# Performance work log

Hardware: AMD Instinct MI355X
Metric: run time of the kernel (lower is better)

## Reference

```python
import jax, jax.numpy as jnp
import numpy as np


def _dequant_linear(x, wq, scale):
    # wq: int [out, in], scale: [out] per-output-channel
    w = wq.astype(jnp.float32) * scale[:, None]  # dequantize
    return jnp.einsum('bsh,oh->bso', x, w)


def setup_inputs() -> dict:
    key = jax.random.key(0)
    ks = jax.random.split(key, 7)
    B, S, H, I = 2, 2048, 4096, 14336
    x = jax.random.normal(ks[0], (B, S, H), dtype=jnp.float32)
    gate_wq = jax.random.randint(ks[1], (I, H), -128, 128, dtype=jnp.int32)
    up_wq = jax.random.randint(ks[2], (I, H), -128, 128, dtype=jnp.int32)
    down_wq = jax.random.randint(ks[3], (H, I), -128, 128, dtype=jnp.int32)
    # small positive per-channel scales (~1/(127*sqrt(fan_in)))
    gate_scale = jax.random.uniform(ks[4], (I,), dtype=jnp.float32, minval=0.5, maxval=1.5) / (127.0 * np.sqrt(H))
    up_scale = jax.random.uniform(ks[5], (I,), dtype=jnp.float32, minval=0.5, maxval=1.5) / (127.0 * np.sqrt(H))
    down_scale = jax.random.uniform(ks[6], (H,), dtype=jnp.float32, minval=0.5, maxval=1.5) / (127.0 * np.sqrt(I))
    return {'x': x, 'gate_wq': gate_wq, 'gate_scale': gate_scale,
            'up_wq': up_wq, 'up_scale': up_scale,
            'down_wq': down_wq, 'down_scale': down_scale}


def reference(x, gate_wq, gate_scale, up_wq, up_scale, down_wq, down_scale):
    gate = _dequant_linear(x, gate_wq, gate_scale)   # [B,S,I]
    up = _dequant_linear(x, up_wq, up_scale)         # [B,S,I]
    h = jax.nn.silu(gate) * up                       # SwiGLU
    return _dequant_linear(h, down_wq, down_scale)   # [B,S,H]
```

## Files before the change

kernel.cpp:

```cpp
#include <hip/hip_runtime.h>

typedef __bf16 bf16x8 __attribute__((ext_vector_type(8)));
typedef float f32x4 __attribute__((ext_vector_type(4)));

__device__ __forceinline__ unsigned short f2bf(float f) {
  unsigned u = __float_as_uint(f);
  u += 0x7FFFu + ((u >> 16) & 1u);
  return (unsigned short)(u >> 16);
}

__device__ __forceinline__ void async16(const void* g, void* l) {
  __builtin_amdgcn_global_load_lds((const __attribute__((address_space(1))) void*)g,
                                   (__attribute__((address_space(3))) void*)l,
                                   16, 0, 0);
}

__global__ void cvt_f32_bf16_k(const float4* __restrict__ in, ushort4* __restrict__ out) {
  int i = blockIdx.x * blockDim.x + threadIdx.x;
  float4 v = in[i];
  ushort4 o;
  o.x = f2bf(v.x); o.y = f2bf(v.y); o.z = f2bf(v.z); o.w = f2bf(v.w);
  out[i] = o;
}

__global__ void cvt_i32_bf16_k(const int4* __restrict__ in, ushort4* __restrict__ out) {
  int i = blockIdx.x * blockDim.x + threadIdx.x;
  int4 v = in[i];
  ushort4 o;
  o.x = f2bf((float)v.x); o.y = f2bf((float)v.y);
  o.z = f2bf((float)v.z); o.w = f2bf((float)v.w);
  out[i] = o;
}

__global__ __launch_bounds__(256, 2)
void gemm_gateup(const unsigned short* __restrict__ A,
                 const unsigned short* __restrict__ Bg,
                 const unsigned short* __restrict__ Bu,
                 const float* __restrict__ gsc, const float* __restrict__ usc,
                 unsigned short* __restrict__ Hout,
                 int M, int N, int K) {
  __shared__ unsigned short sA[128 * 64];
  __shared__ unsigned short sBg[128 * 64];
  __shared__ unsigned short sBu[128 * 64];

  const int tid  = threadIdx.x;
  const int lane = tid & 63;
  const int wv   = tid >> 6;

  const int bid = blockIdx.x;
  const int grp = bid >> 8;
  const int rem = bid & 255;
  const int bN  = ((grp << 3) + (rem & 7)) * 128;
  const int bM  = (rem >> 3) * 128;

  const int srow = lane >> 3;
  const int gcol = ((lane & 7) ^ srow) * 8;

  const unsigned short* gA  = A  + (size_t)(bM + wv * 32 + srow) * K + gcol;
  const unsigned short* gBg = Bg + (size_t)(bN + wv * 32 + srow) * K + gcol;
  const unsigned short* gBu = Bu + (size_t)(bN + wv * 32 + srow) * K + gcol;
  unsigned short* lA  = &sA [(wv * 32) * 64];
  unsigned short* lBg = &sBg[(wv * 32) * 64];
  unsigned short* lBu = &sBu[(wv * 32) * 64];

  const int r  = lane & 15;
  const int q  = lane >> 4;
  const int rx = r & 7;
  const int wm = (wv >> 1) * 64;
  const int wn = (wv & 1) * 64;

  f32x4 accg[4][4], accu[4][4];
#pragma unroll
  for (int i = 0; i < 4; i++)
#pragma unroll
    for (int j = 0; j < 4; j++) {
      accg[i][j] = f32x4{0.f, 0.f, 0.f, 0.f};
      accu[i][j] = f32x4{0.f, 0.f, 0.f, 0.f};
    }

  for (int k0 = 0; k0 < K; k0 += 64) {
    const unsigned short* pA = gA + k0;
    async16(pA,                  lA);
    async16(pA +  8 * (size_t)K, lA +  8 * 64);
    async16(pA + 16 * (size_t)K, lA + 16 * 64);
    async16(pA + 24 * (size_t)K, lA + 24 * 64);
    const unsigned short* pG = gBg + k0;
    async16(pG,                  lBg);
    async16(pG +  8 * (size_t)K, lBg +  8 * 64);
    async16(pG + 16 * (size_t)K, lBg + 16 * 64);
    async16(pG + 24 * (size_t)K, lBg + 24 * 64);
    const unsigned short* pU = gBu + k0;
    async16(pU,                  lBu);
    async16(pU +  8 * (size_t)K, lBu +  8 * 64);
    async16(pU + 16 * (size_t)K, lBu + 16 * 64);
    async16(pU + 24 * (size_t)K, lBu + 24 * 64);
    __syncthreads();

#pragma unroll
    for (int kk = 0; kk < 2; ++kk) {
      const int pc = ((kk * 4 + q) ^ rx) * 8;
      bf16x8 af[4];
#pragma unroll
      for (int mi = 0; mi < 4; mi++)
        af[mi] = *(const bf16x8*)&sA[(wm + mi * 16 + r) * 64 + pc];
#pragma unroll
      for (int ni = 0; ni < 4; ni++) {
        bf16x8 bg = *(const bf16x8*)&sBg[(wn + ni * 16 + r) * 64 + pc];
        bf16x8 bu = *(const bf16x8*)&sBu[(wn + ni * 16 + r) * 64 + pc];
#pragma unroll
        for (int mi = 0; mi < 4; mi++) {
          accg[mi][ni] = __builtin_amdgcn_mfma_f32_16x16x32_bf16(af[mi], bg, accg[mi][ni], 0, 0, 0);
          accu[mi][ni] = __builtin_amdgcn_mfma_f32_16x16x32_bf16(af[mi], bu, accu[mi][ni], 0, 0, 0);
        }
      }
    }
    __syncthreads();
  }

#pragma unroll
  for (int ni = 0; ni < 4; ni++) {
    const int col = bN + wn + ni * 16 + r;
    const float gs = gsc[col], us = usc[col];
#pragma unroll
    for (int mi = 0; mi < 4; mi++) {
#pragma unroll
      for (int rr = 0; rr < 4; rr++) {
        const int row = bM + wm + mi * 16 + q * 4 + rr;
        float g = accg[mi][ni][rr] * gs;
        float u = accu[mi][ni][rr] * us;
        float hv = (g / (1.f + __expf(-g))) * u;
        Hout[(size_t)row * N + col] = f2bf(hv);
      }
    }
  }
}

__global__ __launch_bounds__(256)
void gemm_down(const unsigned short* __restrict__ A,
               const unsigned short* __restrict__ B,
               const float* __restrict__ dsc,
               float* __restrict__ out,
               int M, int N, int K) {
  __shared__ unsigned short sA[128 * 64];
  __shared__ unsigned short sB[128 * 64];

  const int tid  = threadIdx.x;
  const int lane = tid & 63;
  const int wv   = tid >> 6;

  const int bid = blockIdx.x;
  const int grp = bid >> 9;
  const int rem = bid & 511;
  const int bN  = ((grp << 4) + (rem & 15)) * 128;
  const int bM  = (rem >> 4) * 128;

  const int srow = lane >> 3;
  const int gcol = ((lane & 7) ^ srow) * 8;

  const unsigned short* gA = A + (size_t)(bM + wv * 32 + srow) * K + gcol;
  const unsigned short* gB = B + (size_t)(bN + wv * 32 + srow) * K + gcol;
  unsigned short* lA = &sA[(wv * 32) * 64];
  unsigned short* lB = &sB[(wv * 32) * 64];

  const int r  = lane & 15;
  const int q  = lane >> 4;
  const int rx = r & 7;
  const int wm = (wv >> 1) * 64;
  const int wn = (wv & 1) * 64;

  f32x4 acc[4][4];
#pragma unroll
  for (int i = 0; i < 4; i++)
#pragma unroll
    for (int j = 0; j < 4; j++) acc[i][j] = f32x4{0.f, 0.f, 0.f, 0.f};

  for (int k0 = 0; k0 < K; k0 += 64) {
    const unsigned short* pA = gA + k0;
    async16(pA,                  lA);
    async16(pA +  8 * (size_t)K, lA +  8 * 64);
    async16(pA + 16 * (size_t)K, lA + 16 * 64);
    async16(pA + 24 * (size_t)K, lA + 24 * 64);
    const unsigned short* pB = gB + k0;
    async16(pB,                  lB);
    async16(pB +  8 * (size_t)K, lB +  8 * 64);
    async16(pB + 16 * (size_t)K, lB + 16 * 64);
    async16(pB + 24 * (size_t)K, lB + 24 * 64);
    __syncthreads();

#pragma unroll
    for (int kk = 0; kk < 2; ++kk) {
      const int pc = ((kk * 4 + q) ^ rx) * 8;
      bf16x8 af[4];
#pragma unroll
      for (int mi = 0; mi < 4; mi++)
        af[mi] = *(const bf16x8*)&sA[(wm + mi * 16 + r) * 64 + pc];
#pragma unroll
      for (int ni = 0; ni < 4; ni++) {
        bf16x8 bfr = *(const bf16x8*)&sB[(wn + ni * 16 + r) * 64 + pc];
#pragma unroll
        for (int mi = 0; mi < 4; mi++)
          acc[mi][ni] = __builtin_amdgcn_mfma_f32_16x16x32_bf16(af[mi], bfr, acc[mi][ni], 0, 0, 0);
      }
    }
    __syncthreads();
  }

#pragma unroll
  for (int ni = 0; ni < 4; ni++) {
    const int col = bN + wn + ni * 16 + r;
    const float s = dsc[col];
#pragma unroll
    for (int mi = 0; mi < 4; mi++) {
#pragma unroll
      for (int rr = 0; rr < 4; rr++) {
        const int row = bM + wm + mi * 16 + q * 4 + rr;
        out[(size_t)row * N + col] = acc[mi][ni][rr] * s;
      }
    }
  }
}

extern "C" void kernel_launch(void* const* d_in, const int* in_sizes, int n_in,
                              void* d_out, int out_size, void* d_ws, size_t ws_size,
                              hipStream_t stream) {
  constexpr int M  = 4096;
  constexpr int Hd = 4096;
  constexpr int Id = 14336;

  const float* x   = (const float*)d_in[0];
  const int*   gwq = (const int*)  d_in[1];
  const float* gsc = (const float*)d_in[2];
  const int*   uwq = (const int*)  d_in[3];
  const float* usc = (const float*)d_in[4];
  const int*   dwq = (const int*)  d_in[5];
  const float* dsc = (const float*)d_in[6];
  float* out = (float*)d_out;

  unsigned short* xb = (unsigned short*)d_ws;
  unsigned short* w0 = xb + (size_t)M * Hd;
  unsigned short* wu = w0 + (size_t)Id * Hd;
  unsigned short* hb = wu + (size_t)Id * Hd;

  cvt_f32_bf16_k<<<(M * Hd) / 1024, 256, 0, stream>>>((const float4*)x, (ushort4*)xb);
  cvt_i32_bf16_k<<<((size_t)Id * Hd) / 1024, 256, 0, stream>>>((const int4*)gwq, (ushort4*)w0);
  cvt_i32_bf16_k<<<((size_t)Id * Hd) / 1024, 256, 0, stream>>>((const int4*)uwq, (ushort4*)wu);

  gemm_gateup<<<(Id / 128) * (M / 128), 256, 0, stream>>>(xb, w0, wu, gsc, usc, hb, M, Id, Hd);

  cvt_i32_bf16_k<<<((size_t)Hd * Id) / 1024, 256, 0, stream>>>((const int4*)dwq, (ushort4*)w0);

  gemm_down<<<(Hd / 128) * (M / 128), 256, 0, stream>>>(hb, w0, dsc, out, M, Hd, Id);
}
```

Before: 2.219 ms.

## Double-buffer LDS with 8-wave 256-wide tiles and interleaved async staging

New measurement: 2.179 ms. About the same (-1.8%).

```diff
diff --git a/kernel.cpp b/kernel.cpp
--- a/kernel.cpp
+++ b/kernel.cpp
@@ -32,16 +32,43 @@
   out[i] = o;
 }
 
-__global__ __launch_bounds__(256, 2)
+#define BAR() do { asm volatile("" ::: "memory"); __builtin_amdgcn_s_barrier(); \
+                   asm volatile("" ::: "memory"); } while (0)
+
+#define STAGE2(GP, LP) do { async16((GP), (LP)); \
+    async16((GP) + 8 * (size_t)K, (LP) + 8 * 64); } while (0)
+
+#define LOAD_A(AF, CURA, HA)                                                   \
+  _Pragma("unroll") for (int mi = 0; mi < 4; ++mi)                             \
+  _Pragma("unroll") for (int kk = 0; kk < 2; ++kk)                             \
+    AF[mi][kk] = *(const bf16x8*)&(CURA)[((HA) * 128 + wrow + mi * 16 + r) * 64 \
+                                         + (((kk * 4 + q) ^ rx) * 8)];
+
+#define LOAD_B(BF, CURB, HB)                                                   \
+  _Pragma("unroll") for (int ni = 0; ni < 2; ++ni)                             \
+  _Pragma("unroll") for (int kk = 0; kk < 2; ++kk)                             \
+    BF[ni][kk] = *(const bf16x8*)&(CURB)[((HB) * 128 + wcol + ni * 16 + r) * 64 \
+                                         + (((kk * 4 + q) ^ rx) * 8)];
+
+#define MFMA16(ACC, AF, BF)                                                    \
+  __builtin_amdgcn_s_setprio(1);                                               \
+  _Pragma("unroll") for (int kk = 0; kk < 2; ++kk)                             \
+  _Pragma("unroll") for (int ni = 0; ni < 2; ++ni)                             \
+  _Pragma("unroll") for (int mi = 0; mi < 4; ++mi)                             \
+    ACC[mi][ni] = __builtin_amdgcn_mfma_f32_16x16x32_bf16(                     \
+        AF[mi][kk], BF[ni][kk], ACC[mi][ni], 0, 0, 0);                         \
+  __builtin_amdgcn_s_setprio(0);
+
+__global__ __launch_bounds__(512, 2)
 void gemm_gateup(const unsigned short* __restrict__ A,
                  const unsigned short* __restrict__ Bg,
                  const unsigned short* __restrict__ Bu,
                  const float* __restrict__ gsc, const float* __restrict__ usc,
                  unsigned short* __restrict__ Hout,
                  int M, int N, int K) {
-  __shared__ unsigned short sA[128 * 64];
-  __shared__ unsigned short sBg[128 * 64];
-  __shared__ unsigned short sBu[128 * 64];
+  __shared__ unsigned short sA [2 * 256 * 64];
+  __shared__ unsigned short sBg[2 * 128 * 64];
+  __shared__ unsigned short sBu[2 * 128 * 64];
 
   const int tid  = threadIdx.x;
   const int lane = tid & 63;
@@ -50,171 +77,241 @@
   const int bid = blockIdx.x;
   const int grp = bid >> 8;
   const int rem = bid & 255;
-  const int bN  = ((grp << 3) + (rem & 7)) * 128;
-  const int bM  = (rem >> 3) * 128;
+  const int bN  = ((grp << 4) + (rem & 15)) * 128;
+  const int bM  = (rem >> 4) * 256;
 
   const int srow = lane >> 3;
   const int gcol = ((lane & 7) ^ srow) * 8;
 
-  const unsigned short* gA  = A  + (size_t)(bM + wv * 32 + srow) * K + gcol;
-  const unsigned short* gBg = Bg + (size_t)(bN + wv * 32 + srow) * K + gcol;
-  const unsigned short* gBu = Bu + (size_t)(bN + wv * 32 + srow) * K + gcol;
-  unsigned short* lA  = &sA [(wv * 32) * 64];
-  unsigned short* lBg = &sBg[(wv * 32) * 64];
-  unsigned short* lBu = &sBu[(wv * 32) * 64];
-
-  const int r  = lane & 15;
-  const int q  = lane >> 4;
-  const int rx = r & 7;
-  const int wm = (wv >> 1) * 64;
-  const int wn = (wv & 1) * 64;
-
-  f32x4 accg[4][4], accu[4][4];
+  const unsigned short* gA0 = A  + (size_t)(bM +       wv * 16 + srow) * K + gcol;
+  const unsigned short* gA1 = A  + (size_t)(bM + 128 + wv * 16 + srow) * K + gcol;
+  const unsigned short* gBg = Bg + (size_t)(bN +       wv * 16 + srow) * K + gcol;
+  const unsigned short* gBu = Bu + (size_t)(bN +       wv * 16 + srow) * K + gcol;
+
+  const int r    = lane & 15;
+  const int q    = lane >> 4;
+  const int rx   = r & 7;
+  const int wrow = (wv >> 2) * 64;
+  const int wcol = (wv & 3) * 32;
+
+  f32x4 accg0[4][2], accg1[4][2], accu0[4][2], accu1[4][2];
 #pragma unroll
   for (int i = 0; i < 4; i++)
 #pragma unroll
-    for (int j = 0; j < 4; j++) {
-      accg[i][j] = f32x4{0.f, 0.f, 0.f, 0.f};
-      accu[i][j] = f32x4{0.f, 0.f, 0.f, 0.f};
-    }
-
-  for (int k0 = 0; k0 < K; k0 += 64) {
-    const unsigned short* pA = gA + k0;
-    async16(pA,                  lA);
-    async16(pA +  8 * (size_t)K, lA +  8 * 64);
-    async16(pA + 16 * (size_t)K, lA + 16 * 64);
-    async16(pA + 24 * (size_t)K, lA + 24 * 64);
-    const unsigned short* pG = gBg + k0;
-    async16(pG,                  lBg);
-    async16(pG +  8 * (size_t)K, lBg +  8 * 64);
-    async16(pG + 16 * (size_t)K, lBg + 16 * 64);
-    async16(pG + 24 * (size_t)K, lBg + 24 * 64);
-    const unsigned short* pU = gBu + k0;
-    async16(pU,                  lBu);
-    async16(pU +  8 * (size_t)K, lBu +  8 * 64);
-    async16(pU + 16 * (size_t)K, lBu + 16 * 64);
-    async16(pU + 24 * (size_t)K, lBu + 24 * 64);
-    __syncthreads();
-
-#pragma unroll
-    for (int kk = 0; kk < 2; ++kk) {
-      const int pc = ((kk * 4 + q) ^ rx) * 8;
-      bf16x8 af[4];
-#pragma unroll
-      for (int mi = 0; mi < 4; mi++)
-        af[mi] = *(const bf16x8*)&sA[(wm + mi * 16 + r) * 64 + pc];
-#pragma unroll
-      for (int ni = 0; ni < 4; ni++) {
-        bf16x8 bg = *(const bf16x8*)&sBg[(wn + ni * 16 + r) * 64 + pc];
-        bf16x8 bu = *(const bf16x8*)&sBu[(wn + ni * 16 + r) * 64 + pc];
-#pragma unroll
-        for (int mi = 0; mi < 4; mi++) {
-          accg[mi][ni] = __builtin_amdgcn_mfma_f32_16x16x32_bf16(af[mi], bg, accg[mi][ni], 0, 0, 0);
-          accu[mi][ni] = __builtin_amdgcn_mfma_f32_16x16x32_bf16(af[mi], bu, accu[mi][ni], 0, 0, 0);
-        }
+    for (int j = 0; j < 2; j++) {
+      accg0[i][j] = f32x4{0.f, 0.f, 0.f, 0.f};
+      accg1[i][j] = f32x4{0.f, 0.f, 0.f, 0.f};
+      accu0[i][j] = f32x4{0.f, 0.f, 0.f, 0.f};
+      accu1[i][j] = f32x4{0.f, 0.f, 0.f, 0.f};
+    }
+
+  const int NT = K >> 6;
+
+  STAGE2(gA0, &sA [ wv * 16 * 64]);
+  STAGE2(gBg, &sBg[ wv * 16 * 64]);
+  STAGE2(gBu, &sBu[ wv * 16 * 64]);
+  STAGE2(gA1, &sA [(128 + wv * 16) * 64]);
+  asm volatile("s_waitcnt vmcnt(4)" ::: "memory");
+  __builtin_amdgcn_s_barrier();
+
+  int cur = 0;
+  for (int t = 0; t < NT; ++t) {
+    const unsigned short* curA  = sA  + cur * (256 * 64);
+    const unsigned short* curBg = sBg + cur * (128 * 64);
+    const unsigned short* curBu = sBu + cur * (128 * 64);
+    unsigned short* nxtA  = sA  + (cur ^ 1) * (256 * 64);
+    unsigned short* nxtBg = sBg + (cur ^ 1) * (128 * 64);
+    unsigned short* nxtBu = sBu + (cur ^ 1) * (128 * 64);
+    const int  kn = (t + 1) << 6;
+    const bool st = (t + 1) < NT;
+
+    bf16x8 af0[4][2], af1[4][2];
+
+    {
+      bf16x8 bfr[2][2];
+      LOAD_A(af0, curA, 0);
+      LOAD_B(bfr, curBg, 0);
+      if (st) STAGE2(gA0 + kn, nxtA + wv * 16 * 64);
+      BAR();
+      MFMA16(accg0, af0, bfr);
+      if (st) asm volatile("s_waitcnt vmcnt(4)" ::: "memory");
+      else    asm volatile("s_waitcnt vmcnt(2)" ::: "memory");
+      BAR();
+    }
+    {
+      bf16x8 bfr[2][2];
+      LOAD_B(bfr, curBu, 0);
+      if (st) STAGE2(gBg + kn, nxtBg + wv * 16 * 64);
+      BAR();
+      MFMA16(accu0, af0, bfr);
+      if (st) asm volatile("s_waitcnt vmcnt(4)" ::: "memory");
+      else    asm volatile("s_waitcnt vmcnt(0)" ::: "memory");
+      BAR();
+    }
+    {
+      bf16x8 bfr[2][2];
+      LOAD_A(af1, curA, 1);
+      LOAD_B(bfr, curBg, 0);
+      if (st) STAGE2(gBu + kn, nxtBu + wv * 16 * 64);
+      BAR();
+      MFMA16(accg1, af1, bfr);
+      BAR();
+    }
+    {
+      bf16x8 bfr[2][2];
+      LOAD_B(bfr, curBu, 0);
+      if (st) STAGE2(gA1 + kn, nxtA + (128 + wv * 16) * 64);
+      BAR();
+      MFMA16(accu1, af1, bfr);
+      if (st) {
+        asm volatile("s_waitcnt vmcnt(4)" ::: "memory");
+        BAR();
       }
     }
-    __syncthreads();
+    cur ^= 1;
   }
 
 #pragma unroll
-  for (int ni = 0; ni < 4; ni++) {
-    const int col = bN + wn + ni * 16 + r;
+  for (int ni = 0; ni < 2; ++ni) {
+    const int col = bN + wcol + ni * 16 + r;
     const float gs = gsc[col], us = usc[col];
 #pragma unroll
-    for (int mi = 0; mi < 4; mi++) {
-#pragma unroll
-      for (int rr = 0; rr < 4; rr++) {
-        const int row = bM + wm + mi * 16 + q * 4 + rr;
-        float g = accg[mi][ni][rr] * gs;
-        float u = accu[mi][ni][rr] * us;
-        float hv = (g / (1.f + __expf(-g))) * u;
-        Hout[(size_t)row * N + col] = f2bf(hv);
+    for (int mi = 0; mi < 4; ++mi) {
+#pragma unroll
+      for (int rr = 0; rr < 4; ++rr) {
+        const int row0 = bM + wrow + mi * 16 + q * 4 + rr;
+        float g0 = accg0[mi][ni][rr] * gs;
+        float u0 = accu0[mi][ni][rr] * us;
+        Hout[(size_t)row0 * N + col] = f2bf((g0 / (1.f + __expf(-g0))) * u0);
+        const int row1 = row0 + 128;
+        float g1 = accg1[mi][ni][rr] * gs;
+        float u1 = accu1[mi][ni][rr] * us;
+        Hout[(size_t)row1 * N + col] = f2bf((g1 / (1.f + __expf(-g1))) * u1);
       }
     }
   }
 }
 
-__global__ __launch_bounds__(256)
+__global__ __launch_bounds__(512, 2)
 void gemm_down(const unsigned short* __restrict__ A,
                const unsigned short* __restrict__ B,
                const float* __restrict__ dsc,
                float* __restrict__ out,
                int M, int N, int K) {
-  __shared__ unsigned short sA[128 * 64];
-  __shared__ unsigned short sB[128 * 64];
+  __shared__ unsigned short sA[2 * 256 * 64];
+  __shared__ unsigned short sB[2 * 256 * 64];
 
   const int tid  = threadIdx.x;
   const int lane = tid & 63;
   const int wv   = tid >> 6;
 
-  const int bid = blockIdx.x;
-  const int grp = bid >> 9;
-  const int rem = bid & 511;
-  const int bN  = ((grp << 4) + (rem & 15)) * 128;
-  const int bM  = (rem >> 4) * 128;
+  const int bM = (blockIdx.x >> 4) * 256;
+  const int bN = (blockIdx.x & 15) * 256;
 
   const int srow = lane >> 3;
   const int gcol = ((lane & 7) ^ srow) * 8;
 
-  const unsigned short* gA = A + (size_t)(bM + wv * 32 + srow) * K + gcol;
-  const unsigned short* gB = B + (size_t)(bN + wv * 32 + srow) * K + gcol;
-  unsigned short* lA = &sA[(wv * 32) * 64];
-  unsigned short* lB = &sB[(wv * 32) * 64];
-
-  const int r  = lane & 15;
-  const int q  = lane >> 4;
-  const int rx = r & 7;
-  const int wm = (wv >> 1) * 64;
-  const int wn = (wv & 1) * 64;
-
-  f32x4 acc[4][4];
+  const unsigned short* gA0 = A + (size_t)(bM +       wv * 16 + srow) * K + gcol;
+  const unsigned short* gA1 = A + (size_t)(bM + 128 + wv * 16 + srow) * K + gcol;
+  const unsigned short* gB0 = B + (size_t)(bN +       wv * 16 + srow) * K + gcol;
+  const unsigned short* gB1 = B + (size_t)(bN + 128 + wv * 16 + srow) * K + gcol;
+
+  const int r    = lane & 15;
+  const int q    = lane >> 4;
+  const int rx   = r & 7;
+  const int wrow = (wv >> 2) * 64;
+  const int wcol = (wv & 3) * 32;
+
+  f32x4 a00[4][2], a01[4][2], a10[4][2], a11[4][2];
 #pragma unroll
   for (int i = 0; i < 4; i++)
 #pragma unroll
-    for (int j = 0; j < 4; j++) acc[i][j] = f32x4{0.f, 0.f, 0.f, 0.f};
-
-  for (int k0 = 0; k0 < K; k0 += 64) {
-    const unsigned short* pA = gA + k0;
-    async16(pA,                  lA);
-    async16(pA +  8 * (size_t)K, lA +  8 * 64);
-    async16(pA + 16 * (size_t)K, lA + 16 * 64);
-    async16(pA + 24 * (size_t)K, lA + 24 * 64);
-    const unsigned short* pB = gB + k0;
-    async16(pB,                  lB);
-    async16(pB +  8 * (size_t)K, lB +  8 * 64);
-    async16(pB + 16 * (size_t)K, lB + 16 * 64);
-    async16(pB + 24 * (size_t)K, lB + 24 * 64);
-    __syncthreads();
-
-#pragma unroll
-    for (int kk = 0; kk < 2; ++kk) {
-      const int pc = ((kk * 4 + q) ^ rx) * 8;
-      bf16x8 af[4];
-#pragma unroll
-      for (int mi = 0; mi < 4; mi++)
-        af[mi] = *(const bf16x8*)&sA[(wm + mi * 16 + r) * 64 + pc];
-#pragma unroll
-      for (int ni = 0; ni < 4; ni++) {
-        bf16x8 bfr = *(const bf16x8*)&sB[(wn + ni * 16 + r) * 64 + pc];
-#pragma unroll
-        for (int mi = 0; mi < 4; mi++)
-          acc[mi][ni] = __builtin_amdgcn_mfma_f32_16x16x32_bf16(af[mi], bfr, acc[mi][ni], 0, 0, 0);
+    for (int j = 0; j < 2; j++) {
+      a00[i][j] = f32x4{0.f, 0.f, 0.f, 0.f};
+      a01[i][j] = f32x4{0.f, 0.f, 0.f, 0.f};
+      a10[i][j] = f32x4{0.f, 0.f, 0.f, 0.f};
+      a11[i][j] = f32x4{0.f, 0.f, 0.f, 0.f};
+    }
+
+  const int NT = K >> 6;
+
+  STAGE2(gA0, &sA[ wv * 16 * 64]);
+  STAGE2(gB0, &sB[ wv * 16 * 64]);
+  STAGE2(gB1, &sB[(128 + wv * 16) * 64]);
+  STAGE2(gA1, &sA[(128 + wv * 16) * 64]);
+  asm volatile("s_waitcnt vmcnt(4)" ::: "memory");
+  __builtin_amdgcn_s_barrier();
+
+  int cur = 0;
+  for (int t = 0; t < NT; ++t) {
+    const unsigned short* curA = sA + cur * (256 * 64);
+    const unsigned short* curB = sB + cur * (256 * 64);
+    unsigned short* nxtA = sA + (cur ^ 1) * (256 * 64);
+    unsigned short* nxtB = sB + (cur ^ 1) * (256 * 64);
+    const int  kn = (t + 1) << 6;
+    const bool st = (t + 1) < NT;
+
+    bf16x8 af0[4][2], af1[4][2];
+
+    {
+      bf16x8 bfr[2][2];
+      LOAD_A(af0, curA, 0);
+      LOAD_B(bfr, curB, 0);
+      if (st) STAGE2(gA0 + kn, nxtA + wv * 16 * 64);
+      BAR();
+      MFMA16(a00, af0, bfr);
+      if (st) asm volatile("s_waitcnt vmcnt(4)" ::: "memory");
+      else    asm volatile("s_waitcnt vmcnt(2)" ::: "memory");
+      BAR();
+    }
+    {
+      bf16x8 bfr[2][2];
+      LOAD_B(bfr, curB, 1);
+      if (st) STAGE2(gB0 + kn, nxtB + wv * 16 * 64);
+      BAR();
+      MFMA16(a01, af0, bfr);
+      if (st) asm volatile("s_waitcnt vmcnt(4)" ::: "memory");
+      else    asm volatile("s_waitcnt vmcnt(0)" ::: "memory");
+      BAR();
+    }
+    {
+      bf16x8 bfr[2][2];
+      LOAD_A(af1, curA, 1);
+      LOAD_B(bfr, curB, 0);
+      if (st) STAGE2(gB1 + kn, nxtB + (128 + wv * 16) * 64);
+      BAR();
+      MFMA16(a10, af1, bfr);
+      BAR();
+    }
+    {
+      bf16x8 bfr[2][2];
+      LOAD_B(bfr, curB, 1);
+      if (st) STAGE2(gA1 + kn, nxtA + (128 + wv * 16) * 64);
+      BAR();
+      MFMA16(a11, af1, bfr);
+      if (st) {
+        asm volatile("s_waitcnt vmcnt(4)" ::: "memory");
+        BAR();
       }
     }
-    __syncthreads();
+    cur ^= 1;
   }
 
 #pragma unroll
-  for (int ni = 0; ni < 4; ni++) {
-    const int col = bN + wn + ni * 16 + r;
-    const float s = dsc[col];
-#pragma unroll
-    for (int mi = 0; mi < 4; mi++) {
-#pragma unroll
-      for (int rr = 0; rr < 4; rr++) {
-        const int row = bM + wm + mi * 16 + q * 4 + rr;
-        out[(size_t)row * N + col] = acc[mi][ni][rr] * s;
+  for (int ni = 0; ni < 2; ++ni) {
+    const int c0 = bN + wcol + ni * 16 + r;
+    const int c1 = c0 + 128;
+    const float s0 = dsc[c0], s1 = dsc[c1];
+#pragma unroll
+    for (int mi = 0; mi < 4; ++mi) {
+#pragma unroll
+      for (int rr = 0; rr < 4; ++rr) {
+        const int row0 = bM + wrow + mi * 16 + q * 4 + rr;
+        const int row1 = row0 + 128;
+        out[(size_t)row0 * N + c0] = a00[mi][ni][rr] * s0;
+        out[(size_t)row0 * N + c1] = a01[mi][ni][rr] * s1;
+        out[(size_t)row1 * N + c0] = a10[mi][ni][rr] * s0;
+        out[(size_t)row1 * N + c1] = a11[mi][ni][rr] * s1;
       }
     }
   }
@@ -245,9 +342,9 @@
   cvt_i32_bf16_k<<<((size_t)Id * Hd) / 1024, 256, 0, stream>>>((const int4*)gwq, (ushort4*)w0);
   cvt_i32_bf16_k<<<((size_t)Id * Hd) / 1024, 256, 0, stream>>>((const int4*)uwq, (ushort4*)wu);
 
-  gemm_gateup<<<(Id / 128) * (M / 128), 256, 0, stream>>>(xb, w0, wu, gsc, usc, hb, M, Id, Hd);
+  gemm_gateup<<<(M / 256) * (Id / 128), 512, 0, stream>>>(xb, w0, wu, gsc, usc, hb, M, Id, Hd);
 
   cvt_i32_bf16_k<<<((size_t)Hd * Id) / 1024, 256, 0, stream>>>((const int4*)dwq, (ushort4*)w0);
 
-  gemm_down<<<(Hd / 128) * (M / 128), 256, 0, stream>>>(hb, w0, dsc, out, M, Hd, Id);
-}
+  gemm_down<<<(M / 256) * (Hd / 256), 512, 0, stream>>>(hb, w0, dsc, out, M, Hd, Id);
+}
```
